# Kernel tuning notes

Hardware: AMD Instinct MI355X
Metric: run time of the kernel (lower is better)

Reference implementation:

```python
import jax, jax.numpy as jnp
import numpy as np

E = 2048
H = 16
D = E // H  # head_dim = 128
S_SLOTS = 8
EPS = 1e-5


def _linear_params(key, fan_in, fan_out):
    kw, kb = jax.random.split(key)
    lim = 1.0 / np.sqrt(fan_in)
    W = jax.random.uniform(kw, (fan_out, fan_in), jnp.float32, -lim, lim)
    b = jax.random.uniform(kb, (fan_out,), jnp.float32, -lim, lim)
    return W, b


def setup_inputs() -> dict:
    key = jax.random.key(0)
    ks = jax.random.split(key, 10)
    x = jax.random.normal(ks[0], (2, 2048, E), jnp.float32)
    thought_slots = jax.random.normal(ks[1], (S_SLOTS, E), jnp.float32)
    Wq, bq = _linear_params(ks[2], E, E)
    Wk, bk = _linear_params(ks[3], E, E)
    Wv, bv = _linear_params(ks[4], E, E)
    Wtq, btq = _linear_params(ks[5], E, E)
    Wtk, btk = _linear_params(ks[6], E, E)
    Wtv, btv = _linear_params(ks[7], E, E)
    Wo, bo = _linear_params(ks[8], E, E)
    gamma = jnp.ones((E,), jnp.float32)
    beta = jnp.zeros((E,), jnp.float32)
    return dict(x=x, thought_slots=thought_slots, Wq=Wq, bq=bq, Wk=Wk, bk=bk,
                Wv=Wv, bv=bv, Wtq=Wtq, btq=btq, Wtk=Wtk, btk=btk,
                Wtv=Wtv, btv=btv, Wo=Wo, bo=bo, gamma=gamma, beta=beta)


def _heads(t, B):
    # [B, S, E] -> [B, H, S, D]
    return t.reshape(B, -1, H, D).transpose(0, 2, 1, 3)


def reference(x, thought_slots, Wq, bq, Wk, bk, Wv, bv,
              Wtq, btq, Wtk, btk, Wtv, btv, Wo, bo, gamma, beta):
    B, S, _ = x.shape
    scale = 1.0 / np.sqrt(D)

    # regular self-attention stream
    q = _heads(x @ Wq.T + bq, B)
    k = _heads(x @ Wk.T + bk, B)
    v = _heads(x @ Wv.T + bv, B)
    attn = jax.nn.softmax(jnp.einsum('bhqd,bhkd->bhqk', q, k) * scale, axis=-1)
    regular_out = jnp.einsum('bhqk,bhkd->bhqd', attn, v)

    # thought cross-attention stream (keys/values from learned slots)
    slots = jnp.broadcast_to(thought_slots, (B, S_SLOTS, thought_slots.shape[-1]))
    t_q = _heads(x @ Wtq.T + btq, B)
    t_k = _heads(slots @ Wtk.T + btk, B)
    t_v = _heads(slots @ Wtv.T + btv, B)
    t_attn = jax.nn.softmax(jnp.einsum('bhqd,bhkd->bhqk', t_q, t_k) * scale, axis=-1)
    thought_out = jnp.einsum('bhqk,bhkd->bhqd', t_attn, t_v)

    # merge heads, combine, layernorm, output projection
    combined = (regular_out + thought_out).transpose(0, 2, 1, 3).reshape(B, S, E)
    mu = jnp.mean(combined, axis=-1, keepdims=True)
    var = jnp.var(combined, axis=-1, keepdims=True)
    normed = (combined - mu) * jax.lax.rsqrt(var + EPS) * gamma + beta
    return normed @ Wo.T + bo
```

## Files before the change

kernel.cpp:

```cpp
#include <hip/hip_runtime.h>
#include <hip/hip_bf16.h>
#include <stdint.h>

typedef __bf16 bf16;
typedef __bf16 bf16x8 __attribute__((ext_vector_type(8)));
typedef __bf16 bf16x4 __attribute__((ext_vector_type(4)));
typedef float f32x4 __attribute__((ext_vector_type(4)));
typedef float f32x16 __attribute__((ext_vector_type(16)));
typedef uint32_t u32x2 __attribute__((ext_vector_type(2)));
typedef uint32_t u32x4 __attribute__((ext_vector_type(4)));

#define E_DIM 2048
#define HEADS 16
#define HD 128
#define SEQ 2048
#define BATCH 2
#define NTOK 4096
#define NSLOT 8

#define QSCALE (0.08838834764831845f * 1.4426950408889634f)

__device__ __forceinline__ void gload_lds16(const void* g, void* lds) {
  __builtin_amdgcn_global_load_lds(
      (const __attribute__((address_space(1))) uint32_t*)g,
      (__attribute__((address_space(3))) uint32_t*)lds, 16, 0, 0);
}

__global__ __launch_bounds__(256) void cvt_f32_bf16_kernel(
    const float* __restrict__ src, bf16* __restrict__ dst, int n8)
{
  for (int i = blockIdx.x * 256 + threadIdx.x; i < n8; i += gridDim.x * 256) {
    const f32x4 a = *(const f32x4*)(src + i * 8);
    const f32x4 b = *(const f32x4*)(src + i * 8 + 4);
    bf16x8 o;
#pragma unroll
    for (int j = 0; j < 4; j++) { o[j] = (bf16)a[j]; o[4 + j] = (bf16)b[j]; }
    *(bf16x8*)(dst + i * 8) = o;
  }
}

struct ProjArgs {
  const bf16* W[4];
  const float* bias[4];
  void* out[4];
  int mode[4];
  float scale[4];
};

__global__ __launch_bounds__(512, 2) void gemm256_kernel(
    const bf16* __restrict__ A, ProjArgs pa, int nbm, int nbn)
{
  __shared__ bf16 As[2][256 * 64];
  __shared__ bf16 Bs[2][256 * 64];

  const int nwg = gridDim.x;
  const int qch = nwg >> 3;
  const int wg = (blockIdx.x & 7) * qch + (blockIdx.x >> 3);
  const int bm = wg % nbm;
  const int rest = wg / nbm;
  const int bn = rest % nbn;
  const int z = rest / nbn;

  const bf16* __restrict__ W = pa.W[z];
  const float* __restrict__ bias = pa.bias[z];
  void* __restrict__ out = pa.out[z];
  const int mode = pa.mode[z];
  const float scale = pa.scale[z];

  const int tid = threadIdx.x;
  const int lane = tid & 63;
  const int w = tid >> 6;
  const int wr = w >> 2;
  const int wc = w & 3;
  const int g = lane >> 4, c = lane & 15;

  const int rsub = lane >> 3;
  const int csub = ((lane & 7) ^ rsub) * 8;

  const int arow0 = wr * 128 + wc * 32;
  const int hb = wc >> 1, gj = (wr << 1) | (wc & 1);
  const int brow0 = hb * 128 + gj * 32;
  const bf16* Asrc = A + (size_t)(bm * 256 + arow0 + rsub) * 2048 + csub;
  const bf16* Bsrc = W + (size_t)(bn * 256 + brow0 + rsub) * 2048 + csub;

  auto stage = [&](int t, int buf) {
    const int k0 = t * 64;
    char* Adst = (char*)(&As[buf][0]) + arow0 * 128;
    char* Bdst = (char*)(&Bs[buf][0]) + brow0 * 128;
#pragma unroll
    for (int i = 0; i < 4; i++) {
      gload_lds16(Asrc + (size_t)(i * 8) * 2048 + k0, Adst + i * 1024);
      gload_lds16(Bsrc + (size_t)(i * 8) * 2048 + k0, Bdst + i * 1024);
    }
  };

  f32x4 acc[8][4] = {};

  stage(0, 0);
  __syncthreads();
  int cur = 0;

  const int NT = 2048 / 64;
  for (int t = 0; t < NT; t++) {
    if (t + 1 < NT) stage(t + 1, cur ^ 1);
#pragma unroll
    for (int kk = 0; kk < 2; kk++) {
      bf16x8 bfr[4], af[8];
#pragma unroll
      for (int n = 0; n < 4; n++) {
        const int row = wc * 64 + n * 16 + c;
        bfr[n] = *(const bf16x8*)((const char*)(&Bs[cur][0]) + row * 128 +
                                  (((kk * 4 + g) ^ (c & 7)) * 16));
      }
#pragma unroll
      for (int mi = 0; mi < 8; mi++) {
        const int row = wr * 128 + mi * 16 + c;
        af[mi] = *(const bf16x8*)((const char*)(&As[cur][0]) + row * 128 +
                                  (((kk * 4 + g) ^ (c & 7)) * 16));
      }
      __builtin_amdgcn_s_setprio(1);
#pragma unroll
      for (int mi = 0; mi < 8; mi++)
#pragma unroll
        for (int n = 0; n < 4; n++)
          acc[mi][n] = __builtin_amdgcn_mfma_f32_16x16x32_bf16(af[mi], bfr[n], acc[mi][n], 0, 0, 0);
      __builtin_amdgcn_s_setprio(0);
    }
    __syncthreads();
    cur ^= 1;
  }

#pragma unroll
  for (int mi = 0; mi < 8; mi++) {
#pragma unroll
    for (int n = 0; n < 4; n++) {
      const int col = bn * 256 + wc * 64 + n * 16 + c;
      const float bv = bias[col];
#pragma unroll
      for (int j = 0; j < 4; j++) {
        const int row = bm * 256 + wr * 128 + mi * 16 + g * 4 + j;
        const float v = (acc[mi][n][j] + bv) * scale;
        if (mode == 0) {
          ((float*)out)[(size_t)row * E_DIM + col] = v;
        } else {
          const int b = row >> 11, s = row & 2047;
          const int h = col >> 7, d = col & 127;
          size_t idx;
          if (mode == 1) idx = (((size_t)(b * HEADS + h)) * SEQ + s) * HD + d;
          else           idx = (((size_t)(b * HEADS + h)) * HD + d) * SEQ + s;
          ((bf16*)out)[idx] = (bf16)v;
        }
      }
    }
  }
}

__global__ __launch_bounds__(256) void gemm_nt_kernel(
    const bf16* __restrict__ A, ProjArgs pa, int M, int N, int K)
{
  __shared__ bf16 As[2][128 * 32];
  __shared__ bf16 Bs[2][128 * 32];

  const int z = blockIdx.z;
  const bf16* __restrict__ W = pa.W[z];
  const float* __restrict__ bias = pa.bias[z];
  void* __restrict__ out = pa.out[z];
  const int mode = pa.mode[z];
  const float scale = pa.scale[z];

  const int tid = threadIdx.x;
  const int lane = tid & 63;
  const int w = tid >> 6;
  const int wr = w >> 1, wc = w & 1;
  const int g = lane >> 4, c = lane & 15;
  const int bm = blockIdx.x, bn = blockIdx.y;

  f32x4 acc[4][4] = {};

  const int srow = lane >> 2;
  const int scol = (lane & 3) * 8;
  const bf16* Ab = A + (size_t)(bm * 128 + srow) * K + scol;
  const bf16* Wb = W + (size_t)(bn * 128 + srow) * K + scol;

  auto stage = [&](int k0, int buf) {
#pragma unroll
    for (int i = 0; i < 2; ++i) {
      const int chunk = w * 2 + i;
      gload_lds16(Ab + (size_t)(chunk * 16) * K + k0, (char*)(&As[buf][0]) + chunk * 1024);
      gload_lds16(Wb + (size_t)(chunk * 16) * K + k0, (char*)(&Bs[buf][0]) + chunk * 1024);
    }
  };

  stage(0, 0);
  __syncthreads();
  int cur = 0;

  for (int k0 = 0; k0 < K; k0 += 32) {
    if (k0 + 32 < K) stage(k0 + 32, cur ^ 1);
    bf16x8 af[4], bfr[4];
#pragma unroll
    for (int m = 0; m < 4; m++)
      af[m] = *(const bf16x8*)(&As[cur][0] + (wr * 64 + m * 16 + c) * 32 + g * 8);
#pragma unroll
    for (int n = 0; n < 4; n++)
      bfr[n] = *(const bf16x8*)(&Bs[cur][0] + (wc * 64 + n * 16 + c) * 32 + g * 8);
#pragma unroll
    for (int m = 0; m < 4; m++)
#pragma unroll
      for (int n = 0; n < 4; n++)
        acc[m][n] = __builtin_amdgcn_mfma_f32_16x16x32_bf16(af[m], bfr[n], acc[m][n], 0, 0, 0);
    __syncthreads();
    cur ^= 1;
  }

#pragma unroll
  for (int m = 0; m < 4; m++) {
#pragma unroll
    for (int n = 0; n < 4; n++) {
      const int col = bn * 128 + wc * 64 + n * 16 + c;
      const float bv = bias[col];
#pragma unroll
      for (int j = 0; j < 4; j++) {
        const int row = bm * 128 + wr * 64 + m * 16 + g * 4 + j;
        const float v = (acc[m][n][j] + bv) * scale;
        if (mode == 0) {
          ((float*)out)[(size_t)row * N + col] = v;
        } else {
          const int b = row >> 11, s = row & 2047;
          const int h = col >> 7, d = col & 127;
          size_t idx;
          if (mode == 1) idx = (((size_t)(b * HEADS + h)) * SEQ + s) * HD + d;
          else           idx = (((size_t)(b * HEADS + h)) * HD + d) * SEQ + s;
          ((bf16*)out)[idx] = (bf16)v;
        }
      }
    }
  }
}

__global__ __launch_bounds__(256) void slots_proj_kernel(
    const float* __restrict__ slots,
    const float* __restrict__ Wk, const float* __restrict__ bk,
    const float* __restrict__ Wv, const float* __restrict__ bv,
    float* __restrict__ tk, float* __restrict__ tv)
{
  const int col = blockIdx.x * 256 + threadIdx.x;
  const int slot = blockIdx.y;
  const int mat = blockIdx.z;
  const float* W = mat ? Wv : Wk;
  const float* bias = mat ? bv : bk;
  float* out = mat ? tv : tk;
  const float* xr = slots + (size_t)slot * E_DIM;
  const float* wr = W + (size_t)col * E_DIM;
  float acc = 0.f;
  for (int k = 0; k < E_DIM; k += 4) {
    const f32x4 a = *(const f32x4*)(xr + k);
    const f32x4 b4 = *(const f32x4*)(wr + k);
#pragma unroll
    for (int i = 0; i < 4; i++) acc += a[i] * b4[i];
  }
  out[(size_t)slot * E_DIM + col] = acc + bias[col];
}

__global__ __launch_bounds__(512) void flash_attn_kernel(
    const bf16* __restrict__ Qg, const bf16* __restrict__ Kg,
    const bf16* __restrict__ Vtg, bf16* __restrict__ Og)
{
  __shared__ char Ks[2][64 * 256];
  __shared__ char Vs[2][128 * 128];

  const int orig = blockIdx.x;
  const int logical = (orig & 7) * 32 + (orig >> 3);
  const int qt = logical & 7;
  const int bh = logical >> 3;

  const int tid = threadIdx.x;
  const int lane = tid & 63;
  const int w = tid >> 6;
  const int q = lane & 31;
  const int hi = lane >> 5;
  const int b = bh >> 4, h = bh & 15;
  const int q0 = qt * 256 + w * 32;

  const bf16* Qb = Qg + ((size_t)bh * SEQ + q0) * HD;
  const bf16* Kb = Kg + (size_t)bh * SEQ * HD;
  const bf16* Vb = Vtg + (size_t)bh * HD * SEQ;

  auto stage = [&](int kv0, int buf) {
#pragma unroll
    for (int i = 0; i < 2; i++) {
      const int p = (tid + i * 512) * 16;
      { const int r = p >> 8; const int s16 = (p >> 4) & 15;
        gload_lds16(Kb + (size_t)(kv0 + r) * HD + (s16 ^ (r & 15)) * 8, &Ks[buf][0] + p); }
      { const int r = p >> 7; const int s8 = (p >> 4) & 7;
        gload_lds16(Vb + (size_t)r * SEQ + kv0 + (s8 ^ (r & 7)) * 8, &Vs[buf][0] + p); }
    }
  };

  bf16x8 qf[8];
#pragma unroll
  for (int kc = 0; kc < 8; kc++)
    qf[kc] = *(const bf16x8*)(Qb + (size_t)q * HD + kc * 16 + hi * 8);

  stage(0, 0);
  __syncthreads();
  int cur = 0;

  f32x16 o[4] = {};
  float mrun = -1e30f, lsum = 0.f;

  for (int kv0 = 0; kv0 < SEQ; kv0 += 64) {
    if (kv0 + 64 < SEQ) stage(kv0 + 64, cur ^ 1);

    f32x16 st[2] = {};
    __builtin_amdgcn_s_setprio(1);
#pragma unroll
    for (int kc = 0; kc < 8; kc++) {
#pragma unroll
      for (int blk = 0; blk < 2; blk++) {
        const int rt = blk * 32 + q;
        const int sl = (2 * kc + hi) ^ (rt & 15);
        const bf16x8 kf = *(const bf16x8*)(&Ks[cur][0] + rt * 256 + sl * 16);
        st[blk] = __builtin_amdgcn_mfma_f32_32x32x16_bf16(kf, qf[kc], st[blk], 0, 0, 0);
      }
    }
    __builtin_amdgcn_s_setprio(0);

    float t[16];
#pragma unroll
    for (int i = 0; i < 16; i++) t[i] = fmaxf(st[0][i], st[1][i]);
#pragma unroll
    for (int s2 = 8; s2 > 0; s2 >>= 1)
#pragma unroll
      for (int i = 0; i < 8; i++) if (i < s2) t[i] = fmaxf(t[i], t[i + s2]);
    float lm = t[0];
    lm = fmaxf(lm, __shfl_xor(lm, 32));

    float fsc = 1.0f;
    if (__any(lm > mrun + 8.0f)) {
      const float mn = fmaxf(mrun, lm);
      fsc = exp2f(mrun - mn);
      mrun = mn;
#pragma unroll
      for (int db = 0; db < 4; db++)
#pragma unroll
        for (int i = 0; i < 16; i++) o[db][i] *= fsc;
    }

    float ps0 = 0.f, ps1 = 0.f, ps2 = 0.f, ps3 = 0.f;
#pragma unroll
    for (int blk = 0; blk < 2; blk++)
#pragma unroll
      for (int i = 0; i < 16; i += 4) {
        const float p0 = exp2f(st[blk][i]     - mrun);
        const float p1 = exp2f(st[blk][i + 1] - mrun);
        const float p2 = exp2f(st[blk][i + 2] - mrun);
        const float p3 = exp2f(st[blk][i + 3] - mrun);
        st[blk][i] = p0; st[blk][i + 1] = p1; st[blk][i + 2] = p2; st[blk][i + 3] = p3;
        ps0 += p0; ps1 += p1; ps2 += p2; ps3 += p3;
      }
    lsum = lsum * fsc + ((ps0 + ps1) + (ps2 + ps3));

    bf16x8 pb[2][2];
#pragma unroll
    for (int blk = 0; blk < 2; blk++)
#pragma unroll
      for (int c = 0; c < 2; c++) {
        bf16x4 Lv, Hv;
#pragma unroll
        for (int i = 0; i < 4; i++) {
          Lv[i] = (bf16)st[blk][8 * c + i];
          Hv[i] = (bf16)st[blk][8 * c + 4 + i];
        }
        const u32x2 Lu = __builtin_bit_cast(u32x2, Lv);
        const u32x2 Hu = __builtin_bit_cast(u32x2, Hv);
        const uint32_t s0 = hi ? Lu.x : Hu.x;
        const uint32_t s1 = hi ? Lu.y : Hu.y;
        const uint32_t x0 = (uint32_t)__shfl_xor((int)s0, 32);
        const uint32_t x1 = (uint32_t)__shfl_xor((int)s1, 32);
        u32x4 bv;
        bv.x = hi ? x0 : Lu.x;
        bv.y = hi ? x1 : Lu.y;
        bv.z = hi ? Hu.x : x0;
        bv.w = hi ? Hu.y : x1;
        pb[blk][c] = __builtin_bit_cast(bf16x8, bv);
      }

    __builtin_amdgcn_s_setprio(1);
#pragma unroll
    for (int db = 0; db < 4; db++) {
      const int rt = db * 32 + q;
#pragma unroll
      for (int blk = 0; blk < 2; blk++)
#pragma unroll
        for (int c = 0; c < 2; c++) {
          const int sl = (blk * 4 + c * 2 + hi) ^ (rt & 7);
          const bf16x8 vf = *(const bf16x8*)(&Vs[cur][0] + rt * 128 + sl * 16);
          o[db] = __builtin_amdgcn_mfma_f32_32x32x16_bf16(vf, pb[blk][c], o[db], 0, 0, 0);
        }
    }
    __builtin_amdgcn_s_setprio(0);

    __syncthreads();
    cur ^= 1;
  }

  const float lt = lsum + __shfl_xor(lsum, 32);
  const float linv = 1.0f / lt;
  bf16* Orow = Og + ((size_t)b * SEQ + q0 + q) * E_DIM + h * HD;
#pragma unroll
  for (int db = 0; db < 4; db++)
#pragma unroll
    for (int g4 = 0; g4 < 4; g4++) {
      bf16x4 ov;
#pragma unroll
      for (int i = 0; i < 4; i++) ov[i] = (bf16)(o[db][g4 * 4 + i] * linv);
      *(bf16x4*)(Orow + db * 32 + g4 * 8 + hi * 4) = ov;
    }
}

__global__ __launch_bounds__(256) void thought_ln_kernel(
    const bf16* __restrict__ TQ, const float* __restrict__ TK,
    const float* __restrict__ TV, const bf16* __restrict__ ATT,
    const float* __restrict__ gamma, const float* __restrict__ beta,
    bf16* __restrict__ Y)
{
  __shared__ float wsum[4], wsq[4];
  const int tid = threadIdx.x;
  const int lane = tid & 63;
  const int w = tid >> 6;
  const int tok = blockIdx.x;
  const int b = tok >> 11, s = tok & 2047;
  const int e0 = tid * 8;
  const int h = e0 >> 7;
  const int d0 = e0 & 127;

  const bf16x8 av = *(const bf16x8*)(ATT + (size_t)tok * E_DIM + e0);
  float v[8];
#pragma unroll
  for (int i = 0; i < 8; i++) v[i] = (float)av[i];

  const bf16x8 qv8 = *(const bf16x8*)(TQ + (((size_t)(b * HEADS + h)) * SEQ + s) * HD + d0);
  float qv[8];
#pragma unroll
  for (int i = 0; i < 8; i++) qv[i] = (float)qv8[i];

  float dts[NSLOT];
#pragma unroll
  for (int sl = 0; sl < NSLOT; sl++) {
    const float* tkr = TK + (size_t)sl * E_DIM + e0;
    const f32x4 k0 = *(const f32x4*)(tkr);
    const f32x4 k1 = *(const f32x4*)(tkr + 4);
    float dp = 0.f;
#pragma unroll
    for (int i = 0; i < 4; i++) dp += qv[i] * k0[i] + qv[4 + i] * k1[i];
    dp += __shfl_xor(dp, 1);
    dp += __shfl_xor(dp, 2);
    dp += __shfl_xor(dp, 4);
    dp += __shfl_xor(dp, 8);
    dts[sl] = dp;
  }
  float mx = dts[0];
#pragma unroll
  for (int sl = 1; sl < NSLOT; sl++) mx = fmaxf(mx, dts[sl]);
  float p[NSLOT], den = 0.f;
#pragma unroll
  for (int sl = 0; sl < NSLOT; sl++) { p[sl] = exp2f(dts[sl] - mx); den += p[sl]; }
  const float dinv = 1.0f / den;
#pragma unroll
  for (int sl = 0; sl < NSLOT; sl++) {
    const float pn = p[sl] * dinv;
    const float* tvr = TV + (size_t)sl * E_DIM + e0;
    const f32x4 v0 = *(const f32x4*)(tvr);
    const f32x4 v1 = *(const f32x4*)(tvr + 4);
#pragma unroll
    for (int i = 0; i < 4; i++) { v[i] += pn * v0[i]; v[4 + i] += pn * v1[i]; }
  }

  float sm = 0.f, sq = 0.f;
#pragma unroll
  for (int i = 0; i < 8; i++) { sm += v[i]; sq += v[i] * v[i]; }
#pragma unroll
  for (int d = 1; d < 64; d <<= 1) { sm += __shfl_xor(sm, d); sq += __shfl_xor(sq, d); }
  if (lane == 0) { wsum[w] = sm; wsq[w] = sq; }
  __syncthreads();
  const float ts = wsum[0] + wsum[1] + wsum[2] + wsum[3];
  const float tq2 = wsq[0] + wsq[1] + wsq[2] + wsq[3];
  const float mean = ts * (1.f / E_DIM);
  const float var = tq2 * (1.f / E_DIM) - mean * mean;
  const float rstd = rsqrtf(var + 1e-5f);
  const f32x4 g0 = *(const f32x4*)(gamma + e0);
  const f32x4 g1 = *(const f32x4*)(gamma + e0 + 4);
  const f32x4 b0 = *(const f32x4*)(beta + e0);
  const f32x4 b1 = *(const f32x4*)(beta + e0 + 4);
  bf16x8 outv;
#pragma unroll
  for (int i = 0; i < 4; i++) {
    outv[i]     = (bf16)((v[i]     - mean) * rstd * g0[i] + b0[i]);
    outv[4 + i] = (bf16)((v[4 + i] - mean) * rstd * g1[i] + b1[i]);
  }
  *(bf16x8*)(Y + (size_t)tok * E_DIM + e0) = outv;
}

extern "C" void kernel_launch(void* const* d_in, const int* in_sizes, int n_in,
                              void* d_out, int out_size, void* d_ws, size_t ws_size,
                              hipStream_t stream) {
  (void)in_sizes; (void)n_in; (void)out_size; (void)ws_size;
  const float* x     = (const float*)d_in[0];
  const float* slots = (const float*)d_in[1];
  const float* Wq  = (const float*)d_in[2];   const float* bq  = (const float*)d_in[3];
  const float* Wk  = (const float*)d_in[4];   const float* bk  = (const float*)d_in[5];
  const float* Wv  = (const float*)d_in[6];   const float* bv  = (const float*)d_in[7];
  const float* Wtq = (const float*)d_in[8];   const float* btq = (const float*)d_in[9];
  const float* Wtk = (const float*)d_in[10];  const float* btk = (const float*)d_in[11];
  const float* Wtv = (const float*)d_in[12];  const float* btv = (const float*)d_in[13];
  const float* Wo  = (const float*)d_in[14];  const float* bo  = (const float*)d_in[15];
  const float* gamma = (const float*)d_in[16];
  const float* beta  = (const float*)d_in[17];

  uint8_t* ws = (uint8_t*)d_ws;
  const size_t BUF  = (size_t)NTOK * E_DIM * sizeof(bf16);
  const size_t WBUF = (size_t)E_DIM * E_DIM * sizeof(bf16);
  bf16* xb   = (bf16*)(ws + 0 * BUF);
  bf16* qb   = (bf16*)(ws + 1 * BUF);
  bf16* kb   = (bf16*)(ws + 2 * BUF);
  bf16* vtb  = (bf16*)(ws + 3 * BUF);
  bf16* tqb  = (bf16*)(ws + 4 * BUF);
  bf16* attb = (bf16*)(ws + 5 * BUF);
  bf16* nrmb = qb;
  uint8_t* wp = ws + 6 * BUF;
  bf16* Wqb  = (bf16*)(wp + 0 * WBUF);
  bf16* Wkb  = (bf16*)(wp + 1 * WBUF);
  bf16* Wvb  = (bf16*)(wp + 2 * WBUF);
  bf16* Wtqb = (bf16*)(wp + 3 * WBUF);
  bf16* Wob  = (bf16*)(wp + 4 * WBUF);
  float* tkb = (float*)(wp + 5 * WBUF);
  float* tvb = (float*)(wp + 5 * WBUF + 128 * 1024);

  const int WN8 = E_DIM * E_DIM / 8;
  const int XN8 = NTOK * E_DIM / 8;
  cvt_f32_bf16_kernel<<<dim3(2048), 256, 0, stream>>>(x, xb, XN8);
  cvt_f32_bf16_kernel<<<dim3(1024), 256, 0, stream>>>(Wq, Wqb, WN8);
  cvt_f32_bf16_kernel<<<dim3(1024), 256, 0, stream>>>(Wk, Wkb, WN8);
  cvt_f32_bf16_kernel<<<dim3(1024), 256, 0, stream>>>(Wv, Wvb, WN8);
  cvt_f32_bf16_kernel<<<dim3(1024), 256, 0, stream>>>(Wtq, Wtqb, WN8);
  cvt_f32_bf16_kernel<<<dim3(1024), 256, 0, stream>>>(Wo, Wob, WN8);

  ProjArgs pa;
  pa.W[0] = Wqb;  pa.bias[0] = bq;  pa.out[0] = qb;  pa.mode[0] = 1; pa.scale[0] = QSCALE;
  pa.W[1] = Wkb;  pa.bias[1] = bk;  pa.out[1] = kb;  pa.mode[1] = 1; pa.scale[1] = 1.0f;
  pa.W[2] = Wvb;  pa.bias[2] = bv;  pa.out[2] = vtb; pa.mode[2] = 2; pa.scale[2] = 1.0f;
  pa.W[3] = Wtqb; pa.bias[3] = btq; pa.out[3] = tqb; pa.mode[3] = 1; pa.scale[3] = QSCALE;
  gemm256_kernel<<<dim3(16 * 8 * 4), 512, 0, stream>>>(xb, pa, 16, 8);

  slots_proj_kernel<<<dim3(E_DIM / 256, NSLOT, 2), 256, 0, stream>>>(
      slots, Wtk, btk, Wtv, btv, tkb, tvb);

  flash_attn_kernel<<<dim3((SEQ / 256) * BATCH * HEADS), 512, 0, stream>>>(
      qb, kb, vtb, attb);
  thought_ln_kernel<<<dim3(NTOK), 256, 0, stream>>>(
      tqb, tkb, tvb, attb, gamma, beta, nrmb);

  ProjArgs po;
  po.W[0] = Wob; po.bias[0] = bo; po.out[0] = d_out; po.mode[0] = 0; po.scale[0] = 1.0f;
  po.W[1] = po.W[2] = po.W[3] = Wob;
  po.bias[1] = po.bias[2] = po.bias[3] = bo;
  po.out[1] = po.out[2] = po.out[3] = d_out;
  po.mode[1] = po.mode[2] = po.mode[3] = 0;
  po.scale[1] = po.scale[2] = po.scale[3] = 1.0f;
  gemm_nt_kernel<<<dim3(NTOK / 128, E_DIM / 128, 1), 256, 0, stream>>>(
      nrmb, po, NTOK, E_DIM, E_DIM);
}
```

Measured before the change: 455.8 us.

## Deepen GEMM K-pipeline to half-tile stages and shrink flash-attention blocks

The projection GEMM now splits each 64-wide K tile into two 32-wide half-stages spread over four LDS buffers. It issues loads two half-stages ahead and waits with explicit vmcnt counts and raw s_barrier instead of a full __syncthreads per tile, which keeps more global loads in flight while the MFMAs run. Separately, flash attention drops from 512 to 256 threads per block and covers 128 query rows instead of 256, doubling the grid so more blocks can be resident per CU. The trade-off is more complex synchronisation, where a wrong vmcnt count would cause data races, and in attention each K/V tile staged into LDS is reused by fewer query rows.

Result: slower. 549.3 us (+20.5%).

```diff
diff --git a/kernel.cpp b/kernel.cpp
--- a/kernel.cpp
+++ b/kernel.cpp
@@ -20,6 +20,8 @@
 
 #define QSCALE (0.08838834764831845f * 1.4426950408889634f)
 
+#define WAITV(N) asm volatile("s_waitcnt vmcnt(" #N ")" ::: "memory")
+
 __device__ __forceinline__ void gload_lds16(const void* g, void* lds) {
   __builtin_amdgcn_global_load_lds(
       (const __attribute__((address_space(1))) uint32_t*)g,
@@ -50,8 +52,8 @@
 __global__ __launch_bounds__(512, 2) void gemm256_kernel(
     const bf16* __restrict__ A, ProjArgs pa, int nbm, int nbn)
 {
-  __shared__ bf16 As[2][256 * 64];
-  __shared__ bf16 Bs[2][256 * 64];
+  __shared__ char LdsA[2 * 2 * 16384];
+  __shared__ char LdsB[2 * 2 * 16384];
 
   const int nwg = gridDim.x;
   const int qch = nwg >> 3;
@@ -74,49 +76,47 @@
   const int wc = w & 3;
   const int g = lane >> 4, c = lane & 15;
 
-  const int rsub = lane >> 3;
-  const int csub = ((lane & 7) ^ rsub) * 8;
-
-  const int arow0 = wr * 128 + wc * 32;
-  const int hb = wc >> 1, gj = (wr << 1) | (wc & 1);
-  const int brow0 = hb * 128 + gj * 32;
-  const bf16* Asrc = A + (size_t)(bm * 256 + arow0 + rsub) * 2048 + csub;
-  const bf16* Bsrc = W + (size_t)(bn * 256 + brow0 + rsub) * 2048 + csub;
-
-  auto stage = [&](int t, int buf) {
-    const int k0 = t * 64;
-    char* Adst = (char*)(&As[buf][0]) + arow0 * 128;
-    char* Bdst = (char*)(&Bs[buf][0]) + brow0 * 128;
-#pragma unroll
-    for (int i = 0; i < 4; i++) {
-      gload_lds16(Asrc + (size_t)(i * 8) * 2048 + k0, Adst + i * 1024);
-      gload_lds16(Bsrc + (size_t)(i * 8) * 2048 + k0, Bdst + i * 1024);
+  const int rw = tid >> 2;
+  const int sc = ((tid & 3) ^ (rw & 3)) * 8;
+  const bf16* Asrc = A + (size_t)(bm * 256 + rw) * 2048 + sc;
+  const bf16* Bsrc = W + (size_t)(bn * 256 + rw) * 2048 + sc;
+
+  auto stage = [&](int T, int s) {
+    const int q4 = ((T & 1) * 2 + s) * 16384;
+    const int k0 = T * 64 + s * 32;
+#pragma unroll
+    for (int j = 0; j < 2; j++) {
+      gload_lds16(Asrc + (size_t)(j * 128) * 2048 + k0, LdsA + q4 + j * 8192 + tid * 16);
+      gload_lds16(Bsrc + (size_t)(j * 128) * 2048 + k0, LdsB + q4 + j * 8192 + tid * 16);
     }
   };
 
   f32x4 acc[8][4] = {};
 
-  stage(0, 0);
-  __syncthreads();
-  int cur = 0;
+  stage(0, 0); stage(0, 1); stage(1, 0);
+  WAITV(8);
+  __builtin_amdgcn_s_barrier();
 
   const int NT = 2048 / 64;
   for (int t = 0; t < NT; t++) {
-    if (t + 1 < NT) stage(t + 1, cur ^ 1);
-#pragma unroll
-    for (int kk = 0; kk < 2; kk++) {
-      bf16x8 bfr[4], af[8];
+    const int d = t & 1;
+#pragma unroll
+    for (int ph = 0; ph < 2; ph++) {
+      if (ph == 0) { if (t + 1 < NT) stage(t + 1, 1); }
+      else         { if (t + 2 < NT) stage(t + 2, 0); }
+
+      const char* Aq = LdsA + (d * 2 + ph) * 16384;
+      const char* Bq = LdsB + (d * 2 + ph) * 16384;
+      bf16x8 af[8], bfr[4];
 #pragma unroll
       for (int n = 0; n < 4; n++) {
         const int row = wc * 64 + n * 16 + c;
-        bfr[n] = *(const bf16x8*)((const char*)(&Bs[cur][0]) + row * 128 +
-                                  (((kk * 4 + g) ^ (c & 7)) * 16));
+        bfr[n] = *(const bf16x8*)(Bq + row * 64 + ((g ^ (row & 3)) * 16));
       }
 #pragma unroll
       for (int mi = 0; mi < 8; mi++) {
         const int row = wr * 128 + mi * 16 + c;
-        af[mi] = *(const bf16x8*)((const char*)(&As[cur][0]) + row * 128 +
-                                  (((kk * 4 + g) ^ (c & 7)) * 16));
+        af[mi] = *(const bf16x8*)(Aq + row * 64 + ((g ^ (row & 3)) * 16));
       }
       __builtin_amdgcn_s_setprio(1);
 #pragma unroll
@@ -125,9 +125,15 @@
         for (int n = 0; n < 4; n++)
           acc[mi][n] = __builtin_amdgcn_mfma_f32_16x16x32_bf16(af[mi], bfr[n], acc[mi][n], 0, 0, 0);
       __builtin_amdgcn_s_setprio(0);
-    }
-    __syncthreads();
-    cur ^= 1;
+
+      if (ph == 0) {
+        if (t == NT - 1) { WAITV(0); } else { WAITV(8); }
+        __builtin_amdgcn_s_barrier();
+      } else {
+        if (t < NT - 2)       { WAITV(8); __builtin_amdgcn_s_barrier(); }
+        else if (t == NT - 2) { WAITV(4); __builtin_amdgcn_s_barrier(); }
+      }
+    }
   }
 
 #pragma unroll
@@ -144,10 +150,10 @@
           ((float*)out)[(size_t)row * E_DIM + col] = v;
         } else {
           const int b = row >> 11, s = row & 2047;
-          const int h = col >> 7, d = col & 127;
+          const int h = col >> 7, d2 = col & 127;
           size_t idx;
-          if (mode == 1) idx = (((size_t)(b * HEADS + h)) * SEQ + s) * HD + d;
-          else           idx = (((size_t)(b * HEADS + h)) * HD + d) * SEQ + s;
+          if (mode == 1) idx = (((size_t)(b * HEADS + h)) * SEQ + s) * HD + d2;
+          else           idx = (((size_t)(b * HEADS + h)) * HD + d2) * SEQ + s;
           ((bf16*)out)[idx] = (bf16)v;
         }
       }
@@ -262,7 +268,7 @@
   out[(size_t)slot * E_DIM + col] = acc + bias[col];
 }
 
-__global__ __launch_bounds__(512) void flash_attn_kernel(
+__global__ __launch_bounds__(256) void flash_attn_kernel(
     const bf16* __restrict__ Qg, const bf16* __restrict__ Kg,
     const bf16* __restrict__ Vtg, bf16* __restrict__ Og)
 {
@@ -270,9 +276,9 @@
   __shared__ char Vs[2][128 * 128];
 
   const int orig = blockIdx.x;
-  const int logical = (orig & 7) * 32 + (orig >> 3);
-  const int qt = logical & 7;
-  const int bh = logical >> 3;
+  const int logical = (orig & 7) * 64 + (orig >> 3);
+  const int qt = logical & 15;
+  const int bh = logical >> 4;
 
   const int tid = threadIdx.x;
   const int lane = tid & 63;
@@ -280,7 +286,7 @@
   const int q = lane & 31;
   const int hi = lane >> 5;
   const int b = bh >> 4, h = bh & 15;
-  const int q0 = qt * 256 + w * 32;
+  const int q0 = qt * 128 + w * 32;
 
   const bf16* Qb = Qg + ((size_t)bh * SEQ + q0) * HD;
   const bf16* Kb = Kg + (size_t)bh * SEQ * HD;
@@ -288,8 +294,8 @@
 
   auto stage = [&](int kv0, int buf) {
 #pragma unroll
-    for (int i = 0; i < 2; i++) {
-      const int p = (tid + i * 512) * 16;
+    for (int i = 0; i < 4; i++) {
+      const int p = (tid + i * 256) * 16;
       { const int r = p >> 8; const int s16 = (p >> 4) & 15;
         gload_lds16(Kb + (size_t)(kv0 + r) * HD + (s16 ^ (r & 15)) * 8, &Ks[buf][0] + p); }
       { const int r = p >> 7; const int s8 = (p >> 4) & 7;
@@ -365,12 +371,12 @@
 #pragma unroll
     for (int blk = 0; blk < 2; blk++)
 #pragma unroll
-      for (int c = 0; c < 2; c++) {
+      for (int c2 = 0; c2 < 2; c2++) {
         bf16x4 Lv, Hv;
 #pragma unroll
         for (int i = 0; i < 4; i++) {
-          Lv[i] = (bf16)st[blk][8 * c + i];
-          Hv[i] = (bf16)st[blk][8 * c + 4 + i];
+          Lv[i] = (bf16)st[blk][8 * c2 + i];
+          Hv[i] = (bf16)st[blk][8 * c2 + 4 + i];
         }
         const u32x2 Lu = __builtin_bit_cast(u32x2, Lv);
         const u32x2 Hu = __builtin_bit_cast(u32x2, Hv);
@@ -383,7 +389,7 @@
         bv.y = hi ? x1 : Lu.y;
         bv.z = hi ? Hu.x : x0;
         bv.w = hi ? Hu.y : x1;
-        pb[blk][c] = __builtin_bit_cast(bf16x8, bv);
+        pb[blk][c2] = __builtin_bit_cast(bf16x8, bv);
       }
 
     __builtin_amdgcn_s_setprio(1);
@@ -393,10 +399,10 @@
 #pragma unroll
       for (int blk = 0; blk < 2; blk++)
 #pragma unroll
-        for (int c = 0; c < 2; c++) {
-          const int sl = (blk * 4 + c * 2 + hi) ^ (rt & 7);
+        for (int c2 = 0; c2 < 2; c2++) {
+          const int sl = (blk * 4 + c2 * 2 + hi) ^ (rt & 7);
           const bf16x8 vf = *(const bf16x8*)(&Vs[cur][0] + rt * 128 + sl * 16);
-          o[db] = __builtin_amdgcn_mfma_f32_32x32x16_bf16(vf, pb[blk][c], o[db], 0, 0, 0);
+          o[db] = __builtin_amdgcn_mfma_f32_32x32x16_bf16(vf, pb[blk][c2], o[db], 0, 0, 0);
         }
     }
     __builtin_amdgcn_s_setprio(0);
@@ -556,7 +562,7 @@
   slots_proj_kernel<<<dim3(E_DIM / 256, NSLOT, 2), 256, 0, stream>>>(
       slots, Wtk, btk, Wtv, btv, tkb, tvb);
 
-  flash_attn_kernel<<<dim3((SEQ / 256) * BATCH * HEADS), 512, 0, stream>>>(
+  flash_attn_kernel<<<dim3((SEQ / 128) * BATCH * HEADS), 256, 0, stream>>>(
       qb, kb, vtb, attb);
   thought_ln_kernel<<<dim3(NTOK), 256, 0, stream>>>(
       tqb, tkb, tvb, attb, gamma, beta, nrmb);
```
